# Performance work log

Hardware: AMD Instinct MI355X
Metric: run time of the kernel (lower is better)

## Reference

```python
import jax, jax.numpy as jnp
import numpy as np

NUM_LEVELS = 16
BASE_RES = 16
T = 1 << 19            # hashmap size per level (log2_hashmap_size=19)
LEVEL_DIM = 2
SCALE = 2.0 ** (np.log2(2048.0 / 16.0) / (NUM_LEVELS - 1))  # desired_resolution=2048
PRIME1 = 2654435761
PRIME2 = 805459861
N_POINTS = 524288


def hash_encode(x, tables):
    # x: [N,3] in [0,1]; tables: [NUM_LEVELS, T, LEVEL_DIM]
    x = jnp.clip(x, 0.0, 1.0)
    feats = []
    for l in range(NUM_LEVELS):
        R = int(np.ceil(BASE_RES * SCALE ** l))
        pos = x * R                      # grid has R+1 vertices per axis
        p0f = jnp.floor(pos)
        w = pos - p0f                    # trilinear weights [N,3]
        p0 = p0f.astype(jnp.uint32)
        dense = (R + 1) ** 3 <= T
        acc = jnp.zeros((x.shape[0], LEVEL_DIM), dtype=tables.dtype)
        for c in range(8):               # 8 cube corners
            off = np.array([(c >> d) & 1 for d in range(3)], dtype=np.uint32)
            idx = jnp.minimum(p0 + off[None, :], jnp.uint32(R))
            if dense:
                flat = idx[:, 0] + jnp.uint32(R + 1) * idx[:, 1] + jnp.uint32((R + 1) ** 2) * idx[:, 2]
            else:
                flat = idx[:, 0] ^ (idx[:, 1] * jnp.uint32(PRIME1)) ^ (idx[:, 2] * jnp.uint32(PRIME2))
                flat = flat & jnp.uint32(T - 1)
            wc = jnp.prod(jnp.where(off[None, :] == 1, w, 1.0 - w), axis=-1)
            acc = acc + wc[:, None] * tables[l, flat]
        feats.append(acc)
    return jnp.concatenate(feats, axis=-1)  # [N, 32]


def pos_embed(x):
    # NeRF embedding: include input + sin/cos of 2^0..2^5 * x -> 3 + 36 = 39 dims
    outs = [x]
    for j in range(6):
        f = float(2 ** j)
        outs.append(jnp.sin(f * x))
        outs.append(jnp.cos(f * x))
    return jnp.concatenate(outs, axis=-1)


def wn_linear(h, v, g, b):
    # weight-norm: W = g * v / ||v||_row
    w = g[:, None] * v / jnp.linalg.norm(v, axis=1, keepdims=True)
    return h @ w.T + b


def softplus100(x):
    return jax.nn.softplus(100.0 * x) / 100.0


def setup_inputs() -> dict:
    key = jax.random.key(0)
    ks = jax.random.split(key, 8)
    x = jax.random.uniform(ks[0], (N_POINTS, 3), dtype=jnp.float32)
    tables = jax.random.uniform(ks[1], (NUM_LEVELS, T, LEVEL_DIM), minval=-1e-4, maxval=1e-4, dtype=jnp.float32)
    d_in_mlp = 3 + 36 + NUM_LEVELS * LEVEL_DIM  # 71
    dims = [d_in_mlp, 256, 256, 257]
    params = {}
    for l in range(3):
        fan_out = dims[l + 1]
        v = jax.random.normal(ks[2 + l], (dims[l + 1], dims[l]), dtype=jnp.float32) * np.sqrt(2.0 / fan_out)
        params[f'v{l}'] = v
        params[f'g{l}'] = jnp.linalg.norm(v, axis=1)  # weight_norm init: g = ||v||
        params[f'b{l}'] = jnp.zeros((dims[l + 1],), dtype=jnp.float32)
    return {'x': x, 'tables': tables, **params}


def reference(x, tables, v0, g0, b0, v1, g1, b1, v2, g2, b2):
    # object_center=0, object_scale=1, divide_factor=1 -> encoder sees x directly
    feat = hash_encode(x, tables)
    inp = jnp.concatenate([pos_embed(x), feat], axis=-1)  # [N, 71]
    h = softplus100(wn_linear(inp, v0, g0, b0))
    h = softplus100(wn_linear(h, v1, g1, b1))
    return wn_linear(h, v2, g2, b2)  # [N, 257] = sdf(1) + feature(256)
```

## Files before the change

kernel.cpp:

```cpp
#include <hip/hip_runtime.h>
#include <math.h>

typedef __bf16 bf16;
typedef __attribute__((ext_vector_type(8))) __bf16 bf16x8;
typedef __attribute__((ext_vector_type(4))) float f32x4;
typedef __attribute__((ext_vector_type(4))) short s16x4;

#define T_HASH (1u << 19)
#define PRIME1 2654435761u
#define PRIME2 805459861u

struct Levels { unsigned R[16]; unsigned mY[16]; unsigned mZ[16]; unsigned df[16]; };

__device__ __forceinline__ unsigned umin_(unsigned a, unsigned b) { return a < b ? a : b; }

__device__ __forceinline__ int swzoff(int row, int colByte) {
    return row * 512 + (colByte ^ ((row & 7) << 4));
}

__device__ __forceinline__ void stb(char* base, int row, int col, float v) {
    *(bf16*)(base + swzoff(row, col * 2)) = (bf16)v;
}
__device__ __forceinline__ void stw(char* base, int row, int col, unsigned short v) {
    *(unsigned short*)(base + swzoff(row, col * 2)) = v;
}

__device__ __forceinline__ float softplus100f(float v) {
    float u = v * 144.2695041f;
    float e = __builtin_amdgcn_exp2f(u);
    float y = __builtin_amdgcn_logf(1.f + e) * 0.006931471806f;
    return v > 0.25f ? v : y;
}

__device__ __forceinline__ unsigned short f2bfu(float v) {
    bf16 h = (bf16)v;
    return *(unsigned short*)&h;
}

__global__ void prep_weights(const float* __restrict__ v0, const float* __restrict__ g0,
                             const float* __restrict__ v1, const float* __restrict__ g1,
                             const float* __restrict__ v2, const float* __restrict__ g2,
                             unsigned short* __restrict__ W0, unsigned short* __restrict__ W1,
                             unsigned short* __restrict__ W2) {
    int r = blockIdx.x;
    int lane = threadIdx.x;
    const float* src = nullptr; const float* g = nullptr; unsigned short* dst; int K, Kp, row;
    if (r < 256)      { row = r;       src = v0 + row * 71;  g = g0; dst = W0 + row * 96;  K = 71;  Kp = 96;  }
    else if (r < 512) { row = r - 256; src = v1 + row * 256; g = g1; dst = W1 + row * 256; K = 256; Kp = 256; }
    else              { row = r - 512; if (row < 257) { src = v2 + row * 256; g = g2; }
                        dst = W2 + row * 256; K = 256; Kp = 256; }
    float ss = 0.f;
    if (src) for (int c = lane; c < K; c += 64) { float v = src[c]; ss += v * v; }
    for (int off = 32; off; off >>= 1) ss += __shfl_down(ss, off);
    ss = __shfl(ss, 0);
    float scale = src ? (g[row] / sqrtf(ss)) : 0.f;
    for (int c = lane; c < Kp; c += 64) {
        float v = (src && c < K) ? src[c] * scale : 0.f;
        dst[c] = f2bfu(v);
    }
}

__global__ void conv_tables(const float2* __restrict__ t, unsigned* __restrict__ tbf) {
    size_t i = (size_t)blockIdx.x * 256 + threadIdx.x;
    float2 e = t[i];
    tbf[i] = (unsigned)f2bfu(e.x) | ((unsigned)f2bfu(e.y) << 16);
}

__global__ __launch_bounds__(256, 8)
void encode_levels(const float* __restrict__ x, const unsigned* __restrict__ tbf,
                   unsigned* __restrict__ featsLM, Levels lv, int npts) {
    const int slot = blockIdx.x & 7, seq = blockIdx.x >> 3;
    const int l = slot + 8 * (seq & 1);
    const int group = seq >> 1;
    const unsigned Ru = lv.R[l], mY = lv.mY[l], mZ = lv.mZ[l];
    const bool dense = lv.df[l] != 0;
    const unsigned* __restrict__ tl = tbf + (size_t)l * T_HASH;
    unsigned* __restrict__ fout = featsLM + (size_t)l * npts;
    const float Rf = (float)Ru;
    const int base = group * 1024 + threadIdx.x;
#pragma unroll
    for (int k = 0; k < 4; ++k) {
        const int p = base + k * 256;
        float xr0 = x[p * 3 + 0], xr1 = x[p * 3 + 1], xr2 = x[p * 3 + 2];
        const float cx = fminf(fmaxf(xr0, 0.f), 1.f);
        const float cy = fminf(fmaxf(xr1, 0.f), 1.f);
        const float cz = fminf(fmaxf(xr2, 0.f), 1.f);
        float px = cx * Rf, py = cy * Rf, pz = cz * Rf;
        float fx = floorf(px), fy = floorf(py), fz = floorf(pz);
        float wx = px - fx, wy = py - fy, wz = pz - fz;
        unsigned ix = (unsigned)fx, iy = (unsigned)fy, iz = (unsigned)fz;
        unsigned xc0 = ix, xc1 = umin_(ix + 1u, Ru);
        unsigned y0 = iy * mY, y1 = umin_(iy + 1u, Ru) * mY;
        unsigned z0 = iz * mZ, z1 = umin_(iz + 1u, Ru) * mZ;
        unsigned yzA[4] = { y0 + z0, y1 + z0, y0 + z1, y1 + z1 };
        float w0x = 1.f - wx, w0y = 1.f - wy, w0z = 1.f - wz;
        float wyz[4] = { w0y * w0z, wy * w0z, w0y * wz, wy * wz };
        float a0 = 0.f, a1 = 0.f;
#pragma unroll
        for (int c = 0; c < 8; ++c) {
            const int ox = c & 1, cyz = c >> 1;
            unsigned xc = ox ? xc1 : xc0;
            unsigned gi = dense ? (xc + yzA[cyz])
                                : ((xc ^ yzA[cyz]) & (T_HASH - 1u));
            unsigned u = tl[gi];
            float ex = __uint_as_float(u << 16);
            float ey = __uint_as_float(u & 0xffff0000u);
            float wc = (ox ? wx : w0x) * wyz[cyz];
            a0 = fmaf(wc, ex, a0);
            a1 = fmaf(wc, ey, a1);
        }
        unsigned outw = (unsigned)f2bfu(a0) | ((unsigned)f2bfu(a1) << 16);
        __builtin_nontemporal_store(outw, &fout[p]);
    }
}


#define STG_STRIDE 260

template<int KSTEPS, int ROWLEN>
__device__ __forceinline__ void layer_mid(const char* __restrict__ inbuf,
                                          const unsigned short* __restrict__ W,
                                          const float* __restrict__ bias,
                                          char* __restrict__ outbuf, int tid) {
    const int lane = tid & 63, wave = tid >> 6;
    const int lrow = lane & 15, lk = lane >> 4;
    const unsigned short* __restrict__ wrow = W + (wave * 16 + lrow) * ROWLEN + lk * 8;
    f32x4 acc[4] = {};
    bf16x8 abuf[3];
    abuf[0] = *(const bf16x8*)(wrow);
    if (KSTEPS > 1) abuf[1] = *(const bf16x8*)(wrow + 32);
#pragma unroll
    for (int ks = 0; ks < KSTEPS; ++ks) {
        if (ks + 2 < KSTEPS) abuf[(ks + 2) % 3] = *(const bf16x8*)(wrow + (ks + 2) * 32);
        const int k0 = ks * 32 + lk * 8;
        bf16x8 b[4];
#pragma unroll
        for (int pt = 0; pt < 4; ++pt)
            b[pt] = *(const bf16x8*)(inbuf + swzoff(pt * 16 + lrow, k0 * 2));
#pragma unroll
        for (int pt = 0; pt < 4; ++pt)
            acc[pt] = __builtin_amdgcn_mfma_f32_16x16x32_bf16(abuf[ks % 3], b[pt], acc[pt], 0, 0, 0);
    }
    const int c0 = wave * 16 + lk * 4;
    const float4 bv = *(const float4*)(bias + c0);
#pragma unroll
    for (int pt = 0; pt < 4; ++pt) {
        const int p = pt * 16 + lrow;
        s16x4 o;
        o.x = (short)f2bfu(softplus100f(acc[pt][0] + bv.x));
        o.y = (short)f2bfu(softplus100f(acc[pt][1] + bv.y));
        o.z = (short)f2bfu(softplus100f(acc[pt][2] + bv.z));
        o.w = (short)f2bfu(softplus100f(acc[pt][3] + bv.w));
        *(s16x4*)(outbuf + swzoff(p, c0 * 2)) = o;
    }
}

__device__ __forceinline__ void layer_fin(const char* __restrict__ inbuf,
                                          const unsigned short* __restrict__ W2,
                                          const float* __restrict__ b2,
                                          float* __restrict__ stg,
                                          float* __restrict__ out, int tid, int blk) {
    const int lane = tid & 63, wave = tid >> 6;
    const int lrow = lane & 15, lk = lane >> 4;
    const unsigned short* __restrict__ wrow = W2 + (wave * 16 + lrow) * 256 + lk * 8;
    f32x4 acc[4] = {};
    bf16x8 abuf[3];
    abuf[0] = *(const bf16x8*)(wrow);
    abuf[1] = *(const bf16x8*)(wrow + 32);
#pragma unroll
    for (int ks = 0; ks < 8; ++ks) {
        if (ks + 2 < 8) abuf[(ks + 2) % 3] = *(const bf16x8*)(wrow + (ks + 2) * 32);
        const int k0 = ks * 32 + lk * 8;
        bf16x8 b[4];
#pragma unroll
        for (int pt = 0; pt < 4; ++pt)
            b[pt] = *(const bf16x8*)(inbuf + swzoff(pt * 16 + lrow, k0 * 2));
#pragma unroll
        for (int pt = 0; pt < 4; ++pt)
            acc[pt] = __builtin_amdgcn_mfma_f32_16x16x32_bf16(abuf[ks % 3], b[pt], acc[pt], 0, 0, 0);
    }
    const int p = tid >> 4, sub = tid & 15;
    float part = 0.f;
    {
        const unsigned short* __restrict__ w2r = W2 + 256 * 256 + sub * 16;
        bf16x8 h0 = *(const bf16x8*)(inbuf + swzoff(p, sub * 32));
        bf16x8 h1 = *(const bf16x8*)(inbuf + swzoff(p, sub * 32 + 16));
        bf16x8 w0 = *(const bf16x8*)(w2r);
        bf16x8 w1 = *(const bf16x8*)(w2r + 8);
#pragma unroll
        for (int j = 0; j < 8; ++j) {
            part = fmaf((float)h0[j], (float)w0[j], part);
            part = fmaf((float)h1[j], (float)w1[j], part);
        }
    }
#pragma unroll
    for (int m = 1; m < 16; m <<= 1) part += __shfl_xor(part, m);

    __syncthreads();
    const int c0 = wave * 16 + lk * 4;
    const float4 bv = *(const float4*)(b2 + c0);
#pragma unroll
    for (int pt = 0; pt < 4; ++pt) {
        const int pr = pt * 16 + lrow;
        f32x4 v;
        v[0] = acc[pt][0] + bv.x;
        v[1] = acc[pt][1] + bv.y;
        v[2] = acc[pt][2] + bv.z;
        v[3] = acc[pt][3] + bv.w;
        *(f32x4*)(stg + pr * STG_STRIDE + c0) = v;
    }
    if (sub == 0) stg[p * STG_STRIDE + 256] = part + b2[256];
    __syncthreads();
    float* __restrict__ dst = out + (size_t)blk * 16448;
#pragma unroll
    for (int r = 0; r < 4; ++r) {
        const int f0 = (r * 1024 + tid) * 4;
        const unsigned pp = ((unsigned)f0 * 65281u) >> 24;
        const int cc = f0 - (int)pp * 257;
        f32x4 v;
#pragma unroll
        for (int u = 0; u < 4; ++u) {
            int c2 = cc + u; unsigned p2 = pp;
            if (c2 >= 257) { c2 -= 257; p2++; }
            v[u] = stg[p2 * STG_STRIDE + c2];
        }
        *(f32x4*)(dst + f0) = v;
    }
    if (tid < 64) {
        const int f0 = 16384 + tid;
        const unsigned pp = ((unsigned)f0 * 65281u) >> 24;
        const int cc = f0 - (int)pp * 257;
        dst[f0] = stg[pp * STG_STRIDE + cc];
    }
}

template<bool SPLIT>
__global__ __launch_bounds__(1024, 8)
void fused_net(const float* __restrict__ x, const float2* __restrict__ tables,
               const unsigned* __restrict__ featsLM,
               const unsigned short* __restrict__ W0, const unsigned short* __restrict__ W1,
               const unsigned short* __restrict__ W2,
               const float* __restrict__ b0, const float* __restrict__ b1, const float* __restrict__ b2,
               float* __restrict__ out, Levels lv, int npts) {
    __shared__ __align__(16) char smem[66560 + 256];
    unsigned* sR  = (unsigned*)(smem + 66560);
    unsigned* sMY = sR + 16;
    unsigned* sMZ = sR + 32;
    unsigned* sDF = sR + 48;
    char* buf0 = smem;
    char* buf1 = smem + 32768;
    float* stg = (float*)smem;
    const int tid = threadIdx.x;
    const int blk = blockIdx.x;

    if (!SPLIT) {
        if (tid >= 960) {
            int i = tid - 960;
            if (i < 16)      sR[i]  = lv.R[i];
            else if (i < 32) sMY[i - 16] = lv.mY[i - 16];
            else if (i < 48) sMZ[i - 32] = lv.mZ[i - 32];
            else             sDF[i - 48] = lv.df[i - 48];
        }
        __syncthreads();
    }

    const int p = tid >> 4, sub = tid & 15;
    const float xr0 = x[(size_t)blk * 192 + p * 3 + 0];
    const float xr1 = x[(size_t)blk * 192 + p * 3 + 1];
    const float xr2 = x[(size_t)blk * 192 + p * 3 + 2];

    if (sub < 13) {
        int c0 = sub * 3;
#pragma unroll
        for (int u = 0; u < 3; ++u) {
            int c = c0 + u;
            if (c >= 39) break;
            float v;
            if (c < 3) v = (c == 0) ? xr0 : (c == 1 ? xr1 : xr2);
            else {
                int q = c - 3, j = q / 6, k = q - j * 6;
                int axis = (k < 3) ? k : k - 3;
                float xv = axis == 0 ? xr0 : (axis == 1 ? xr1 : xr2);
                float fx = (float)(1 << j) * xv;
                v = (k < 3) ? __sinf(fx) : __cosf(fx);
            }
            stb(buf0, p, c, v);
        }
    }
    for (int c = 71 + sub; c < 96; c += 16) stb(buf0, p, c, 0.f);

    if (SPLIT) {
        const int l = sub;
        unsigned u = featsLM[(size_t)l * npts + blk * 64 + p];
        stw(buf0, p, 39 + 2 * l, (unsigned short)(u & 0xffffu));
        stw(buf0, p, 40 + 2 * l, (unsigned short)(u >> 16));
    } else {
        const int l = sub;
        const float cx = fminf(fmaxf(xr0, 0.f), 1.f);
        const float cy = fminf(fmaxf(xr1, 0.f), 1.f);
        const float cz = fminf(fmaxf(xr2, 0.f), 1.f);
        const unsigned Ru = sR[l], mY = sMY[l], mZ = sMZ[l];
        const bool dense = sDF[l] != 0;
        const unsigned lofs = (unsigned)l << 19;
        const float Rf = (float)Ru;
        float px = cx * Rf, py = cy * Rf, pz = cz * Rf;
        float fx = floorf(px), fy = floorf(py), fz = floorf(pz);
        float wx = px - fx, wy = py - fy, wz = pz - fz;
        unsigned ix = (unsigned)fx, iy = (unsigned)fy, iz = (unsigned)fz;
        unsigned xc0 = ix, xc1 = umin_(ix + 1u, Ru);
        unsigned y0 = iy * mY, y1 = umin_(iy + 1u, Ru) * mY;
        unsigned z0 = iz * mZ, z1 = umin_(iz + 1u, Ru) * mZ;
        unsigned yzA[4] = { y0 + z0 + lofs, y1 + z0 + lofs, y0 + z1 + lofs, y1 + z1 + lofs };
        unsigned yzX[4] = { y0 ^ z0, y1 ^ z0, y0 ^ z1, y1 ^ z1 };
        float w0x = 1.f - wx, w0y = 1.f - wy, w0z = 1.f - wz;
        float wyz[4] = { w0y * w0z, wy * w0z, w0y * wz, wy * wz };
        float a0 = 0.f, a1 = 0.f;
#pragma unroll
        for (int c = 0; c < 8; ++c) {
            const int ox = c & 1, cyz = c >> 1;
            unsigned xc = ox ? xc1 : xc0;
            unsigned fd = xc + yzA[cyz];
            unsigned fh = ((xc ^ yzX[cyz]) & (T_HASH - 1u)) + lofs;
            unsigned gi = dense ? fd : fh;
            float2 e2 = tables[gi];
            float wc = (ox ? wx : w0x) * wyz[cyz];
            a0 = fmaf(wc, e2.x, a0);
            a1 = fmaf(wc, e2.y, a1);
        }
        stb(buf0, p, 39 + 2 * l, a0);
        stb(buf0, p, 40 + 2 * l, a1);
    }
    __syncthreads();

    layer_mid<3, 96>(buf0, W0, b0, buf1, tid);
    __syncthreads();
    layer_mid<8, 256>(buf1, W1, b1, buf0, tid);
    __syncthreads();
    layer_fin(buf0, W2, b2, stg, out, tid, blk);
}

extern "C" void kernel_launch(void* const* d_in, const int* in_sizes, int n_in,
                              void* d_out, int out_size, void* d_ws, size_t ws_size,
                              hipStream_t stream) {
    const float*  x      = (const float*)d_in[0];
    const float2* tables = (const float2*)d_in[1];
    const float*  v0 = (const float*)d_in[2];
    const float*  g0 = (const float*)d_in[3];
    const float*  b0 = (const float*)d_in[4];
    const float*  v1 = (const float*)d_in[5];
    const float*  g1 = (const float*)d_in[6];
    const float*  b1 = (const float*)d_in[7];
    const float*  v2 = (const float*)d_in[8];
    const float*  g2 = (const float*)d_in[9];
    const float*  b2 = (const float*)d_in[10];

    unsigned short* W0 = (unsigned short*)d_ws;
    unsigned short* W1 = W0 + 256 * 96;
    unsigned short* W2 = W1 + 256 * 256;
    size_t ofs_tbf   = 319488;
    size_t ofs_feats = ofs_tbf + (size_t)16 * T_HASH * 4;
    size_t need      = ofs_feats + (size_t)16 * T_HASH * 4;
    unsigned* tbf     = (unsigned*)((char*)d_ws + ofs_tbf);
    unsigned* featsLM = (unsigned*)((char*)d_ws + ofs_feats);
    bool use_split = ws_size >= need;

    Levels lv;
    double SCALE = pow(2.0, log2(2048.0 / 16.0) / 15.0);
    for (int l = 0; l < 16; ++l) {
        double r = 16.0 * pow(SCALE, (double)l);
        unsigned R = (unsigned)ceil(r);
        lv.R[l] = R;
        unsigned long long s = (unsigned long long)R + 1;
        int dense = (s * s * s <= (unsigned long long)T_HASH) ? 1 : 0;
        lv.df[l] = dense;
        lv.mY[l] = dense ? (R + 1u) : PRIME1;
        lv.mZ[l] = dense ? (R + 1u) * (R + 1u) : PRIME2;
    }

    prep_weights<<<784, 64, 0, stream>>>(v0, g0, v1, g1, v2, g2, W0, W1, W2);

    int n = in_sizes[0] / 3;
    int nblk = n / 64;

    if (use_split) {
        conv_tables<<<16 * T_HASH / 256, 256, 0, stream>>>(tables, tbf);
        encode_levels<<<8 * (n / 1024) * 2, 256, 0, stream>>>(x, tbf, featsLM, lv, n);
        fused_net<true><<<nblk, 1024, 0, stream>>>(x, tables, featsLM, W0, W1, W2,
                                                   b0, b1, b2, (float*)d_out, lv, n);
    } else {
        fused_net<false><<<nblk, 1024, 0, stream>>>(x, tables, nullptr, W0, W1, W2,
                                                    b0, b1, b2, (float*)d_out, lv, n);
    }
}
```

Baseline: 625.2 us.

## Halve block size to 512 threads, each wave computes two 16-row output tiles

Blocks drop from 1024 to 512 threads while still covering 64 points per block. In each MLP layer a wave now computes 32 output columns as two 16-row MFMA tiles, so each B fragment read from LDS feeds two MFMAs. The encoding, pos-embed and final-layer dot product are remapped so each thread handles two hash levels and more columns. This cuts LDS reads per MFMA and thread count per block, at the cost of more registers per thread, fewer waves to hide the latency of hash-table gathers, and a changed launch bound.

```diff
diff --git a/kernel.cpp b/kernel.cpp
--- a/kernel.cpp
+++ b/kernel.cpp
@@ -124,14 +124,19 @@
                                           char* __restrict__ outbuf, int tid) {
     const int lane = tid & 63, wave = tid >> 6;
     const int lrow = lane & 15, lk = lane >> 4;
-    const unsigned short* __restrict__ wrow = W + (wave * 16 + lrow) * ROWLEN + lk * 8;
-    f32x4 acc[4] = {};
-    bf16x8 abuf[3];
-    abuf[0] = *(const bf16x8*)(wrow);
-    if (KSTEPS > 1) abuf[1] = *(const bf16x8*)(wrow + 32);
+    const unsigned short* __restrict__ wr0 = W + (wave * 32 + lrow) * ROWLEN + lk * 8;
+    const unsigned short* __restrict__ wr1 = wr0 + 16 * ROWLEN;
+    f32x4 acc[2][4] = {};
+    bf16x8 a0[3], a1[3];
+    a0[0] = *(const bf16x8*)(wr0);
+    a1[0] = *(const bf16x8*)(wr1);
+    if (KSTEPS > 1) { a0[1] = *(const bf16x8*)(wr0 + 32); a1[1] = *(const bf16x8*)(wr1 + 32); }
 #pragma unroll
     for (int ks = 0; ks < KSTEPS; ++ks) {
-        if (ks + 2 < KSTEPS) abuf[(ks + 2) % 3] = *(const bf16x8*)(wrow + (ks + 2) * 32);
+        if (ks + 2 < KSTEPS) {
+            a0[(ks + 2) % 3] = *(const bf16x8*)(wr0 + (ks + 2) * 32);
+            a1[(ks + 2) % 3] = *(const bf16x8*)(wr1 + (ks + 2) * 32);
+        }
         const int k0 = ks * 32 + lk * 8;
         bf16x8 b[4];
 #pragma unroll
@@ -139,19 +144,25 @@
             b[pt] = *(const bf16x8*)(inbuf + swzoff(pt * 16 + lrow, k0 * 2));
 #pragma unroll
         for (int pt = 0; pt < 4; ++pt)
-            acc[pt] = __builtin_amdgcn_mfma_f32_16x16x32_bf16(abuf[ks % 3], b[pt], acc[pt], 0, 0, 0);
-    }
-    const int c0 = wave * 16 + lk * 4;
-    const float4 bv = *(const float4*)(bias + c0);
-#pragma unroll
-    for (int pt = 0; pt < 4; ++pt) {
-        const int p = pt * 16 + lrow;
-        s16x4 o;
-        o.x = (short)f2bfu(softplus100f(acc[pt][0] + bv.x));
-        o.y = (short)f2bfu(softplus100f(acc[pt][1] + bv.y));
-        o.z = (short)f2bfu(softplus100f(acc[pt][2] + bv.z));
-        o.w = (short)f2bfu(softplus100f(acc[pt][3] + bv.w));
-        *(s16x4*)(outbuf + swzoff(p, c0 * 2)) = o;
+            acc[0][pt] = __builtin_amdgcn_mfma_f32_16x16x32_bf16(a0[ks % 3], b[pt], acc[0][pt], 0, 0, 0);
+#pragma unroll
+        for (int pt = 0; pt < 4; ++pt)
+            acc[1][pt] = __builtin_amdgcn_mfma_f32_16x16x32_bf16(a1[ks % 3], b[pt], acc[1][pt], 0, 0, 0);
+    }
+#pragma unroll
+    for (int mr = 0; mr < 2; ++mr) {
+        const int c0 = wave * 32 + mr * 16 + lk * 4;
+        const float4 bv = *(const float4*)(bias + c0);
+#pragma unroll
+        for (int pt = 0; pt < 4; ++pt) {
+            const int p = pt * 16 + lrow;
+            s16x4 o;
+            o.x = (short)f2bfu(softplus100f(acc[mr][pt][0] + bv.x));
+            o.y = (short)f2bfu(softplus100f(acc[mr][pt][1] + bv.y));
+            o.z = (short)f2bfu(softplus100f(acc[mr][pt][2] + bv.z));
+            o.w = (short)f2bfu(softplus100f(acc[mr][pt][3] + bv.w));
+            *(s16x4*)(outbuf + swzoff(p, c0 * 2)) = o;
+        }
     }
 }
 
@@ -162,14 +173,20 @@
                                           float* __restrict__ out, int tid, int blk) {
     const int lane = tid & 63, wave = tid >> 6;
     const int lrow = lane & 15, lk = lane >> 4;
-    const unsigned short* __restrict__ wrow = W2 + (wave * 16 + lrow) * 256 + lk * 8;
-    f32x4 acc[4] = {};
-    bf16x8 abuf[3];
-    abuf[0] = *(const bf16x8*)(wrow);
-    abuf[1] = *(const bf16x8*)(wrow + 32);
+    const unsigned short* __restrict__ wr0 = W2 + (wave * 32 + lrow) * 256 + lk * 8;
+    const unsigned short* __restrict__ wr1 = wr0 + 16 * 256;
+    f32x4 acc[2][4] = {};
+    bf16x8 a0[3], a1[3];
+    a0[0] = *(const bf16x8*)(wr0);
+    a1[0] = *(const bf16x8*)(wr1);
+    a0[1] = *(const bf16x8*)(wr0 + 32);
+    a1[1] = *(const bf16x8*)(wr1 + 32);
 #pragma unroll
     for (int ks = 0; ks < 8; ++ks) {
-        if (ks + 2 < 8) abuf[(ks + 2) % 3] = *(const bf16x8*)(wrow + (ks + 2) * 32);
+        if (ks + 2 < 8) {
+            a0[(ks + 2) % 3] = *(const bf16x8*)(wr0 + (ks + 2) * 32);
+            a1[(ks + 2) % 3] = *(const bf16x8*)(wr1 + (ks + 2) * 32);
+        }
         const int k0 = ks * 32 + lk * 8;
         bf16x8 b[4];
 #pragma unroll
@@ -177,44 +194,53 @@
             b[pt] = *(const bf16x8*)(inbuf + swzoff(pt * 16 + lrow, k0 * 2));
 #pragma unroll
         for (int pt = 0; pt < 4; ++pt)
-            acc[pt] = __builtin_amdgcn_mfma_f32_16x16x32_bf16(abuf[ks % 3], b[pt], acc[pt], 0, 0, 0);
-    }
-    const int p = tid >> 4, sub = tid & 15;
+            acc[0][pt] = __builtin_amdgcn_mfma_f32_16x16x32_bf16(a0[ks % 3], b[pt], acc[0][pt], 0, 0, 0);
+#pragma unroll
+        for (int pt = 0; pt < 4; ++pt)
+            acc[1][pt] = __builtin_amdgcn_mfma_f32_16x16x32_bf16(a1[ks % 3], b[pt], acc[1][pt], 0, 0, 0);
+    }
+    const int p = tid >> 3, sub = tid & 7;
     float part = 0.f;
     {
-        const unsigned short* __restrict__ w2r = W2 + 256 * 256 + sub * 16;
-        bf16x8 h0 = *(const bf16x8*)(inbuf + swzoff(p, sub * 32));
-        bf16x8 h1 = *(const bf16x8*)(inbuf + swzoff(p, sub * 32 + 16));
-        bf16x8 w0 = *(const bf16x8*)(w2r);
-        bf16x8 w1 = *(const bf16x8*)(w2r + 8);
-#pragma unroll
-        for (int j = 0; j < 8; ++j) {
-            part = fmaf((float)h0[j], (float)w0[j], part);
-            part = fmaf((float)h1[j], (float)w1[j], part);
-        }
-    }
-#pragma unroll
-    for (int m = 1; m < 16; m <<= 1) part += __shfl_xor(part, m);
+        const unsigned short* __restrict__ w2r = W2 + 256 * 256 + sub * 32;
+#pragma unroll
+        for (int q = 0; q < 2; ++q) {
+            bf16x8 h0 = *(const bf16x8*)(inbuf + swzoff(p, sub * 64 + q * 32));
+            bf16x8 h1 = *(const bf16x8*)(inbuf + swzoff(p, sub * 64 + q * 32 + 16));
+            bf16x8 w0 = *(const bf16x8*)(w2r + q * 16);
+            bf16x8 w1 = *(const bf16x8*)(w2r + q * 16 + 8);
+#pragma unroll
+            for (int j = 0; j < 8; ++j) {
+                part = fmaf((float)h0[j], (float)w0[j], part);
+                part = fmaf((float)h1[j], (float)w1[j], part);
+            }
+        }
+    }
+#pragma unroll
+    for (int m = 1; m < 8; m <<= 1) part += __shfl_xor(part, m);
 
     __syncthreads();
-    const int c0 = wave * 16 + lk * 4;
-    const float4 bv = *(const float4*)(b2 + c0);
-#pragma unroll
-    for (int pt = 0; pt < 4; ++pt) {
-        const int pr = pt * 16 + lrow;
-        f32x4 v;
-        v[0] = acc[pt][0] + bv.x;
-        v[1] = acc[pt][1] + bv.y;
-        v[2] = acc[pt][2] + bv.z;
-        v[3] = acc[pt][3] + bv.w;
-        *(f32x4*)(stg + pr * STG_STRIDE + c0) = v;
+#pragma unroll
+    for (int mr = 0; mr < 2; ++mr) {
+        const int c0 = wave * 32 + mr * 16 + lk * 4;
+        const float4 bv = *(const float4*)(b2 + c0);
+#pragma unroll
+        for (int pt = 0; pt < 4; ++pt) {
+            const int pr = pt * 16 + lrow;
+            f32x4 v;
+            v[0] = acc[mr][pt][0] + bv.x;
+            v[1] = acc[mr][pt][1] + bv.y;
+            v[2] = acc[mr][pt][2] + bv.z;
+            v[3] = acc[mr][pt][3] + bv.w;
+            *(f32x4*)(stg + pr * STG_STRIDE + c0) = v;
+        }
     }
     if (sub == 0) stg[p * STG_STRIDE + 256] = part + b2[256];
     __syncthreads();
     float* __restrict__ dst = out + (size_t)blk * 16448;
 #pragma unroll
-    for (int r = 0; r < 4; ++r) {
-        const int f0 = (r * 1024 + tid) * 4;
+    for (int r = 0; r < 8; ++r) {
+        const int f0 = (r * 512 + tid) * 4;
         const unsigned pp = ((unsigned)f0 * 65281u) >> 24;
         const int cc = f0 - (int)pp * 257;
         f32x4 v;
@@ -235,7 +261,7 @@
 }
 
 template<bool SPLIT>
-__global__ __launch_bounds__(1024, 8)
+__global__ __launch_bounds__(512, 4)
 void fused_net(const float* __restrict__ x, const float2* __restrict__ tables,
                const unsigned* __restrict__ featsLM,
                const unsigned short* __restrict__ W0, const unsigned short* __restrict__ W1,
@@ -254,8 +280,8 @@
     const int blk = blockIdx.x;
 
     if (!SPLIT) {
-        if (tid >= 960) {
-            int i = tid - 960;
+        if (tid >= 448) {
+            int i = tid - 448;
             if (i < 16)      sR[i]  = lv.R[i];
             else if (i < 32) sMY[i - 16] = lv.mY[i - 16];
             else if (i < 48) sMZ[i - 32] = lv.mZ[i - 32];
@@ -264,17 +290,15 @@
         __syncthreads();
     }
 
-    const int p = tid >> 4, sub = tid & 15;
+    const int p = tid >> 3, sub = tid & 7;
     const float xr0 = x[(size_t)blk * 192 + p * 3 + 0];
     const float xr1 = x[(size_t)blk * 192 + p * 3 + 1];
     const float xr2 = x[(size_t)blk * 192 + p * 3 + 2];
 
-    if (sub < 13) {
-        int c0 = sub * 3;
-#pragma unroll
-        for (int u = 0; u < 3; ++u) {
-            int c = c0 + u;
-            if (c >= 39) break;
+    {
+        int c0 = sub * 5;
+        int ce = c0 + 5; if (ce > 39) ce = 39;
+        for (int c = c0; c < ce; ++c) {
             float v;
             if (c < 3) v = (c == 0) ? xr0 : (c == 1 ? xr1 : xr2);
             else {
@@ -287,48 +311,54 @@
             stb(buf0, p, c, v);
         }
     }
-    for (int c = 71 + sub; c < 96; c += 16) stb(buf0, p, c, 0.f);
+    for (int c = 71 + sub; c < 96; c += 8) stb(buf0, p, c, 0.f);
 
     if (SPLIT) {
-        const int l = sub;
-        unsigned u = featsLM[(size_t)l * npts + blk * 64 + p];
-        stw(buf0, p, 39 + 2 * l, (unsigned short)(u & 0xffffu));
-        stw(buf0, p, 40 + 2 * l, (unsigned short)(u >> 16));
+#pragma unroll
+        for (int t = 0; t < 2; ++t) {
+            const int l = sub * 2 + t;
+            unsigned u = featsLM[(size_t)l * npts + blk * 64 + p];
+            stw(buf0, p, 39 + 2 * l, (unsigned short)(u & 0xffffu));
+            stw(buf0, p, 40 + 2 * l, (unsigned short)(u >> 16));
+        }
     } else {
-        const int l = sub;
         const float cx = fminf(fmaxf(xr0, 0.f), 1.f);
         const float cy = fminf(fmaxf(xr1, 0.f), 1.f);
         const float cz = fminf(fmaxf(xr2, 0.f), 1.f);
-        const unsigned Ru = sR[l], mY = sMY[l], mZ = sMZ[l];
-        const bool dense = sDF[l] != 0;
-        const unsigned lofs = (unsigned)l << 19;
-        const float Rf = (float)Ru;
-        float px = cx * Rf, py = cy * Rf, pz = cz * Rf;
-        float fx = floorf(px), fy = floorf(py), fz = floorf(pz);
-        float wx = px - fx, wy = py - fy, wz = pz - fz;
-        unsigned ix = (unsigned)fx, iy = (unsigned)fy, iz = (unsigned)fz;
-        unsigned xc0 = ix, xc1 = umin_(ix + 1u, Ru);
-        unsigned y0 = iy * mY, y1 = umin_(iy + 1u, Ru) * mY;
-        unsigned z0 = iz * mZ, z1 = umin_(iz + 1u, Ru) * mZ;
-        unsigned yzA[4] = { y0 + z0 + lofs, y1 + z0 + lofs, y0 + z1 + lofs, y1 + z1 + lofs };
-        unsigned yzX[4] = { y0 ^ z0, y1 ^ z0, y0 ^ z1, y1 ^ z1 };
-        float w0x = 1.f - wx, w0y = 1.f - wy, w0z = 1.f - wz;
-        float wyz[4] = { w0y * w0z, wy * w0z, w0y * wz, wy * wz };
-        float a0 = 0.f, a1 = 0.f;
-#pragma unroll
-        for (int c = 0; c < 8; ++c) {
-            const int ox = c & 1, cyz = c >> 1;
-            unsigned xc = ox ? xc1 : xc0;
-            unsigned fd = xc + yzA[cyz];
-            unsigned fh = ((xc ^ yzX[cyz]) & (T_HASH - 1u)) + lofs;
-            unsigned gi = dense ? fd : fh;
-            float2 e2 = tables[gi];
-            float wc = (ox ? wx : w0x) * wyz[cyz];
-            a0 = fmaf(wc, e2.x, a0);
-            a1 = fmaf(wc, e2.y, a1);
-        }
-        stb(buf0, p, 39 + 2 * l, a0);
-        stb(buf0, p, 40 + 2 * l, a1);
+#pragma unroll
+        for (int t = 0; t < 2; ++t) {
+            const int l = sub * 2 + t;
+            const unsigned Ru = sR[l], mY = sMY[l], mZ = sMZ[l];
+            const bool dense = sDF[l] != 0;
+            const unsigned lofs = (unsigned)l << 19;
+            const float Rf = (float)Ru;
+            float px = cx * Rf, py = cy * Rf, pz = cz * Rf;
+            float fx = floorf(px), fy = floorf(py), fz = floorf(pz);
+            float wx = px - fx, wy = py - fy, wz = pz - fz;
+            unsigned ix = (unsigned)fx, iy = (unsigned)fy, iz = (unsigned)fz;
+            unsigned xc0 = ix, xc1 = umin_(ix + 1u, Ru);
+            unsigned y0 = iy * mY, y1 = umin_(iy + 1u, Ru) * mY;
+            unsigned z0 = iz * mZ, z1 = umin_(iz + 1u, Ru) * mZ;
+            unsigned yzA[4] = { y0 + z0 + lofs, y1 + z0 + lofs, y0 + z1 + lofs, y1 + z1 + lofs };
+            unsigned yzX[4] = { y0 ^ z0, y1 ^ z0, y0 ^ z1, y1 ^ z1 };
+            float w0x = 1.f - wx, w0y = 1.f - wy, w0z = 1.f - wz;
+            float wyz[4] = { w0y * w0z, wy * w0z, w0y * wz, wy * wz };
+            float a0 = 0.f, a1 = 0.f;
+#pragma unroll
+            for (int c = 0; c < 8; ++c) {
+                const int ox = c & 1, cyz = c >> 1;
+                unsigned xc = ox ? xc1 : xc0;
+                unsigned fd = xc + yzA[cyz];
+                unsigned fh = ((xc ^ yzX[cyz]) & (T_HASH - 1u)) + lofs;
+                unsigned gi = dense ? fd : fh;
+                float2 e2 = tables[gi];
+                float wc = (ox ? wx : w0x) * wyz[cyz];
+                a0 = fmaf(wc, e2.x, a0);
+                a1 = fmaf(wc, e2.y, a1);
+            }
+            stb(buf0, p, 39 + 2 * l, a0);
+            stb(buf0, p, 40 + 2 * l, a1);
+        }
     }
     __syncthreads();
 
@@ -385,10 +415,10 @@
     if (use_split) {
         conv_tables<<<16 * T_HASH / 256, 256, 0, stream>>>(tables, tbf);
         encode_levels<<<8 * (n / 1024) * 2, 256, 0, stream>>>(x, tbf, featsLM, lv, n);
-        fused_net<true><<<nblk, 1024, 0, stream>>>(x, tables, featsLM, W0, W1, W2,
+        fused_net<true><<<nblk, 512, 0, stream>>>(x, tables, featsLM, W0, W1, W2,
+                                                  b0, b1, b2, (float*)d_out, lv, n);
+    } else {
+        fused_net<false><<<nblk, 512, 0, stream>>>(x, tables, nullptr, W0, W1, W2,
                                                    b0, b1, b2, (float*)d_out, lv, n);
-    } else {
-        fused_net<false><<<nblk, 1024, 0, stream>>>(x, tables, nullptr, W0, W1, W2,
-                                                    b0, b1, b2, (float*)d_out, lv, n);
-    }
-}
+    }
+}
```

After: 644.2 us. +3.0%, slower.

## Store hash tables as scaled FP8 and coalesce feature loads in fused net

Applied to the files above, without the earlier changes.

The converted hash tables are stored as scaled FP8 pairs, two bytes per entry instead of four. This halves the table footprint so more of it fits in cache for the random gathers, and it halves the conversion write traffic. Entries are multiplied by 8192 before conversion and the accumulated features are multiplied by its inverse afterwards. FP8 keeps only about 3 mantissa bits, so feature precision drops well below bf16, which risks going past the accuracy tolerance. Separately, the feature load in the fused net is remapped so that each wave reads one level's 64 consecutive points, making those global loads coalesced.

```diff
diff --git a/kernel.cpp b/kernel.cpp
--- a/kernel.cpp
+++ b/kernel.cpp
@@ -9,6 +9,8 @@
 #define T_HASH (1u << 19)
 #define PRIME1 2654435761u
 #define PRIME2 805459861u
+#define FP8_SCALE 8192.0f
+#define FP8_INV   (1.0f / 8192.0f)
 
 struct Levels { unsigned R[16]; unsigned mY[16]; unsigned mZ[16]; unsigned df[16]; };
 
@@ -60,21 +62,22 @@
     }
 }
 
-__global__ void conv_tables(const float2* __restrict__ t, unsigned* __restrict__ tbf) {
+__global__ void conv_tables(const float2* __restrict__ t, unsigned short* __restrict__ tf8) {
     size_t i = (size_t)blockIdx.x * 256 + threadIdx.x;
     float2 e = t[i];
-    tbf[i] = (unsigned)f2bfu(e.x) | ((unsigned)f2bfu(e.y) << 16);
+    int pk = __builtin_amdgcn_cvt_pk_fp8_f32(e.x * FP8_SCALE, e.y * FP8_SCALE, 0, false);
+    tf8[i] = (unsigned short)(pk & 0xffff);
 }
 
 __global__ __launch_bounds__(256, 8)
-void encode_levels(const float* __restrict__ x, const unsigned* __restrict__ tbf,
+void encode_levels(const float* __restrict__ x, const unsigned short* __restrict__ tf8,
                    unsigned* __restrict__ featsLM, Levels lv, int npts) {
     const int slot = blockIdx.x & 7, seq = blockIdx.x >> 3;
     const int l = slot + 8 * (seq & 1);
     const int group = seq >> 1;
     const unsigned Ru = lv.R[l], mY = lv.mY[l], mZ = lv.mZ[l];
     const bool dense = lv.df[l] != 0;
-    const unsigned* __restrict__ tl = tbf + (size_t)l * T_HASH;
+    const unsigned short* __restrict__ tl = tf8 + (size_t)l * T_HASH;
     unsigned* __restrict__ fout = featsLM + (size_t)l * npts;
     const float Rf = (float)Ru;
     const int base = group * 1024 + threadIdx.x;
@@ -102,13 +105,14 @@
             unsigned xc = ox ? xc1 : xc0;
             unsigned gi = dense ? (xc + yzA[cyz])
                                 : ((xc ^ yzA[cyz]) & (T_HASH - 1u));
-            unsigned u = tl[gi];
-            float ex = __uint_as_float(u << 16);
-            float ey = __uint_as_float(u & 0xffff0000u);
+            unsigned u = (unsigned)tl[gi];
+            float ex = __builtin_amdgcn_cvt_f32_fp8(u, 0);
+            float ey = __builtin_amdgcn_cvt_f32_fp8(u, 1);
             float wc = (ox ? wx : w0x) * wyz[cyz];
             a0 = fmaf(wc, ex, a0);
             a1 = fmaf(wc, ey, a1);
         }
+        a0 *= FP8_INV; a1 *= FP8_INV;
         unsigned outw = (unsigned)f2bfu(a0) | ((unsigned)f2bfu(a1) << 16);
         __builtin_nontemporal_store(outw, &fout[p]);
     }
@@ -269,6 +273,13 @@
     const float xr1 = x[(size_t)blk * 192 + p * 3 + 1];
     const float xr2 = x[(size_t)blk * 192 + p * 3 + 2];
 
+    if (SPLIT) {
+        const int l = tid >> 6, pt = tid & 63;
+        unsigned u = featsLM[(size_t)l * npts + blk * 64 + pt];
+        stw(buf0, pt, 39 + 2 * l, (unsigned short)(u & 0xffffu));
+        stw(buf0, pt, 40 + 2 * l, (unsigned short)(u >> 16));
+    }
+
     if (sub < 13) {
         int c0 = sub * 3;
 #pragma unroll
@@ -289,12 +300,7 @@
     }
     for (int c = 71 + sub; c < 96; c += 16) stb(buf0, p, c, 0.f);
 
-    if (SPLIT) {
-        const int l = sub;
-        unsigned u = featsLM[(size_t)l * npts + blk * 64 + p];
-        stw(buf0, p, 39 + 2 * l, (unsigned short)(u & 0xffffu));
-        stw(buf0, p, 40 + 2 * l, (unsigned short)(u >> 16));
-    } else {
+    if (!SPLIT) {
         const int l = sub;
         const float cx = fminf(fmaxf(xr0, 0.f), 1.f);
         const float cy = fminf(fmaxf(xr1, 0.f), 1.f);
@@ -357,11 +363,11 @@
     unsigned short* W0 = (unsigned short*)d_ws;
     unsigned short* W1 = W0 + 256 * 96;
     unsigned short* W2 = W1 + 256 * 256;
-    size_t ofs_tbf   = 319488;
-    size_t ofs_feats = ofs_tbf + (size_t)16 * T_HASH * 4;
+    size_t ofs_tf8   = 319488;
+    size_t ofs_feats = ofs_tf8 + (size_t)16 * T_HASH * 2;
     size_t need      = ofs_feats + (size_t)16 * T_HASH * 4;
-    unsigned* tbf     = (unsigned*)((char*)d_ws + ofs_tbf);
-    unsigned* featsLM = (unsigned*)((char*)d_ws + ofs_feats);
+    unsigned short* tf8 = (unsigned short*)((char*)d_ws + ofs_tf8);
+    unsigned* featsLM   = (unsigned*)((char*)d_ws + ofs_feats);
     bool use_split = ws_size >= need;
 
     Levels lv;
@@ -383,8 +389,8 @@
     int nblk = n / 64;
 
     if (use_split) {
-        conv_tables<<<16 * T_HASH / 256, 256, 0, stream>>>(tables, tbf);
-        encode_levels<<<8 * (n / 1024) * 2, 256, 0, stream>>>(x, tbf, featsLM, lv, n);
+        conv_tables<<<16 * T_HASH / 256, 256, 0, stream>>>(tables, tf8);
+        encode_levels<<<8 * (n / 1024) * 2, 256, 0, stream>>>(x, tf8, featsLM, lv, n);
         fused_net<true><<<nblk, 1024, 0, stream>>>(x, tables, featsLM, W0, W1, W2,
                                                    b0, b1, b2, (float*)d_out, lv, n);
     } else {
```

New measurement: 579.7 us (median of 2 runs). 7.3% less time.
